# Optimization experiments

Hardware: AMD Instinct MI355X
Metric: run time of the kernel (lower is better)

## Reference

```python
import jax, jax.numpy as jnp
import numpy as np

MARGIN = 5.0
VAR_FLOOR = 1e-4
BIG = 1e6


def setup_inputs() -> dict:
    key = jax.random.key(0)
    ks = jax.random.split(key, 8)
    B, D, R = 512, 768, 128
    C_new, C_old = 10, 100
    return {
        "features": jax.random.normal(ks[0], (B, D), jnp.float32),
        "labels": jax.random.randint(ks[1], (B,), 0, C_new),
        "new_class_ids": jnp.arange(C_new),
        "cur_means": jax.random.normal(ks[2], (C_new, D), jnp.float32),
        "cur_bases": jax.random.normal(ks[3], (C_new, D, R), jnp.float32),
        "cur_variances": jax.random.uniform(ks[4], (C_new, R + 1), jnp.float32),
        "calibrated_old_means": jax.random.normal(ks[5], (C_old, D), jnp.float32),
        "calibrated_old_bases": jax.random.normal(ks[6], (C_old, D, R), jnp.float32),
        "calibrated_old_variances": jax.random.uniform(ks[7], (C_old, R + 1), jnp.float32),
    }


def _geometry_distance_matrix(z, means, bases, variances):
    # z: [B,D], means: [C,D], bases: [C,D,R], variances: [C,R+1] -> [B,C]
    diff = z[:, None, :] - means[None, :, :]                    # [B,C,D]
    coeff = jnp.einsum('bcd,cdr->bcr', diff, bases)             # [B,C,R]
    eig = jnp.maximum(variances[:, :-1], VAR_FLOOR)             # [C,R]
    res = jnp.maximum(variances[:, -1], VAR_FLOOR)              # [C]
    parallel = jnp.sum(coeff * coeff / eig[None, :, :], axis=-1)  # [B,C]
    recon = jnp.einsum('bcr,cdr->bcd', coeff, bases)            # [B,C,D]
    residual_term = jnp.sum((diff - recon) ** 2, axis=-1) / res[None, :]
    dist = (parallel + residual_term) / z.shape[1]              # normalize_by_dim
    return jnp.nan_to_num(dist, nan=BIG, posinf=BIG, neginf=BIG)


def reference(features, labels, new_class_ids, cur_means, cur_bases, cur_variances,
              calibrated_old_means, calibrated_old_bases, calibrated_old_variances):
    z = jnp.nan_to_num(features, nan=0.0, posinf=0.0, neginf=0.0)  # [B,D]
    labels = labels.reshape(-1)

    own_all = _geometry_distance_matrix(z, cur_means, cur_bases, cur_variances)  # [B,C_new_total]
    old_all = _geometry_distance_matrix(z, calibrated_old_means, calibrated_old_bases,
                                        calibrated_old_variances)               # [B,C_old]
    old_min = jnp.min(old_all, axis=1)                                           # [B]

    # Per-new-class masks; union of class masks reproduces new_mask implicitly.
    masks = (labels[None, :] == new_class_ids[:, None]).astype(z.dtype)          # [K,B]
    counts = masks.sum(axis=1)                                                   # [K]
    denom = jnp.maximum(counts, 1.0)

    own_k = own_all[:, new_class_ids].T                                          # [K,B]
    hinge = jax.nn.relu(MARGIN + own_k - old_min[None, :])                       # [K,B]

    total_k = (hinge * masks).sum(axis=1) / denom
    own_k_mean = (own_k * masks).sum(axis=1) / denom
    old_k_mean = (old_min[None, :] * masks).sum(axis=1) / denom

    valid = (counts > 0).astype(z.dtype)
    n_valid = jnp.maximum(valid.sum(), 1.0)
    total = (total_k * valid).sum() / n_valid
    own = (own_k_mean * valid).sum() / n_valid
    old = (old_k_mean * valid).sum() / n_valid
    return jnp.stack([total, own, old])  # [total, own, old]
```

## Files before the change

kernel.cpp:

```cpp
#include <hip/hip_runtime.h>
#include <hip/hip_bf16.h>
#include <math.h>
#include <stdint.h>

#define B_N   512
#define D_N   768
#define R_N   128
#define C_NEW 10
#define C_OLD 100
#define C_TOT 110
#define MARGIN_F    5.0f
#define VAR_FLOOR_F 1e-4f
#define BIG_F       1e6f

typedef __bf16 bf16;
typedef __bf16 bf16x4 __attribute__((ext_vector_type(4)));
typedef __bf16 bf16x8 __attribute__((ext_vector_type(8)));
typedef float  f32x4  __attribute__((ext_vector_type(4)));

__device__ __forceinline__ float cleanf(float v) { return isfinite(v) ? v : 0.0f; }

__device__ __forceinline__ void gld16(const bf16* g, bf16* l) {
    __builtin_amdgcn_global_load_lds(
        (const __attribute__((address_space(1))) unsigned int*)g,
        (__attribute__((address_space(3))) unsigned int*)l, 16, 0, 0);
}

__global__ __launch_bounds__(256)
void prep_z(const float* __restrict__ z, bf16* __restrict__ zbf, float* __restrict__ znorm)
{
    const int wave = threadIdx.x >> 6, lane = threadIdx.x & 63;
    const int b = blockIdx.x * 4 + wave;
    const float4* src = (const float4*)(z + (size_t)b * D_N);
    bf16x4* dst = (bf16x4*)(zbf + (size_t)b * D_N);
    float nrm = 0.f;
    #pragma unroll
    for (int i = 0; i < 3; ++i) {
        float4 v = src[lane + i * 64];
        v.x = cleanf(v.x); v.y = cleanf(v.y); v.z = cleanf(v.z); v.w = cleanf(v.w);
        nrm += v.x * v.x + v.y * v.y + v.z * v.z + v.w * v.w;
        bf16x4 w;
        w[0] = (bf16)v.x; w[1] = (bf16)v.y; w[2] = (bf16)v.z; w[3] = (bf16)v.w;
        dst[lane + i * 64] = w;
    }
    #pragma unroll
    for (int off = 32; off >= 1; off >>= 1) nrm += __shfl_xor(nrm, off, 64);
    if (lane == 0) znorm[b] = nrm;
}

__global__ __launch_bounds__(256)
void prep_bases(const float* __restrict__ cur_bases, const float* __restrict__ old_bases,
                const float* __restrict__ cur_means, const float* __restrict__ old_means,
                bf16* __restrict__ basesT, bf16* __restrict__ G,
                float* __restrict__ m_c, float* __restrict__ munorm)
{
    const int c = blockIdx.x;
    const float* Bc = (c < C_NEW) ? cur_bases + (size_t)c * D_N * R_N
                                  : old_bases + (size_t)(c - C_NEW) * D_N * R_N;
    const float* mu = (c < C_NEW) ? cur_means + (size_t)c * D_N
                                  : old_means + (size_t)(c - C_NEW) * D_N;

    __shared__ bf16 T[128][136];
    __shared__ float sMu[D_N];
    __shared__ float sRed[256];

    const int tid = threadIdx.x, wave = tid >> 6, lane = tid & 63;
    const int quad = lane >> 4, l15 = lane & 15;
    const int wr = (wave >> 1) * 64, wcn = (wave & 1) * 64;

    float mn = 0.f;
    for (int i = tid; i < D_N; i += 256) { float v = mu[i]; sMu[i] = v; mn += v * v; }
    #pragma unroll
    for (int off = 32; off >= 1; off >>= 1) mn += __shfl_xor(mn, off, 64);
    if (lane == 0) sRed[wave] = mn;
    __syncthreads();
    if (tid == 0) munorm[c] = sRed[0] + sRed[1] + sRed[2] + sRed[3];

    float mcAcc = 0.f;
    const int mr = tid & 127, mdh = tid >> 7;

    f32x4 acc[4][4];
    #pragma unroll
    for (int i = 0; i < 4; ++i)
        #pragma unroll
        for (int j = 0; j < 4; ++j) acc[i][j] = (f32x4)0.0f;

    for (int ch = 0; ch < 6; ++ch) {
        const int d0 = ch * 128;
        __syncthreads();
        #pragma unroll
        for (int m = 0; m < 2; ++m) {
            int u = m * 256 + tid;
            int r4 = (u & 31) * 4;
            int dg = u >> 5;
            float4 v[8];
            #pragma unroll
            for (int j = 0; j < 8; ++j)
                v[j] = *(const float4*)(Bc + (size_t)(d0 + dg * 8 + j) * R_N + r4);
            #pragma unroll
            for (int i = 0; i < 4; ++i) {
                bf16x8 w;
                #pragma unroll
                for (int j = 0; j < 8; ++j) {
                    float f = (i == 0) ? v[j].x : (i == 1) ? v[j].y : (i == 2) ? v[j].z : v[j].w;
                    w[j] = (bf16)f;
                }
                *(bf16x8*)&T[r4 + i][dg * 8] = w;
            }
        }
        __syncthreads();
        {
            int r = tid >> 1, hf = tid & 1;
            const uint4* srcp = (const uint4*)&T[r][hf * 64];
            uint4* dstp = (uint4*)(basesT + (size_t)c * R_N * D_N + (size_t)r * D_N + d0 + hf * 64);
            #pragma unroll
            for (int m2 = 0; m2 < 8; ++m2) dstp[m2] = srcp[m2];
        }
        #pragma unroll 8
        for (int k = 0; k < 64; ++k)
            mcAcc += sMu[d0 + mdh * 64 + k] * (float)T[mr][mdh * 64 + k];
        #pragma unroll
        for (int kk = 0; kk < 128; kk += 32) {
            bf16x8 af[4], bg[4];
            #pragma unroll
            for (int i = 0; i < 4; ++i) af[i] = *(const bf16x8*)&T[wr + 16 * i + l15][kk + quad * 8];
            #pragma unroll
            for (int j = 0; j < 4; ++j) bg[j] = *(const bf16x8*)&T[wcn + 16 * j + l15][kk + quad * 8];
            #pragma unroll
            for (int i = 0; i < 4; ++i)
                #pragma unroll
                for (int j = 0; j < 4; ++j)
                    acc[i][j] = __builtin_amdgcn_mfma_f32_16x16x32_bf16(af[i], bg[j], acc[i][j], 0, 0, 0);
        }
    }
    __syncthreads();
    sRed[tid] = mcAcc;
    __syncthreads();
    if (tid < 128) m_c[c * R_N + tid] = sRed[tid] + sRed[128 + tid];

    #pragma unroll
    for (int i = 0; i < 4; ++i)
        #pragma unroll
        for (int j = 0; j < 4; ++j)
            #pragma unroll
            for (int reg = 0; reg < 4; ++reg) {
                int r = wr + 16 * i + quad * 4 + reg;
                int s = wcn + 16 * j + l15;
                G[(size_t)c * 16384 + (size_t)r * 128 + s] = (bf16)acc[i][j][reg];
            }
}

#define PADC 136
#define SM_AB  0
#define SM_C   32768
#define SM_M   67584
#define SM_INV 68096
#define SM_PAR 68608
#define SM_CN  69120
#define SM_Q   69632
#define SM_T2  70144
#define SM_MU  73216
#define SM_SZ  74752

__global__ __launch_bounds__(256, 2)
void main_dist(const bf16* __restrict__ zbf, const bf16* __restrict__ basesT,
               const bf16* __restrict__ G, const float* __restrict__ m_c,
               const float* __restrict__ cur_vars, const float* __restrict__ old_vars,
               const float* __restrict__ cur_means, const float* __restrict__ old_means,
               const float* __restrict__ znorm, const float* __restrict__ munorm,
               float* __restrict__ gdist)
{
    const int mt = blockIdx.x, c = blockIdx.y;
    const int b0 = mt * 128;
    const float* vars = (c < C_NEW) ? cur_vars + (size_t)c * (R_N + 1)
                                    : old_vars + (size_t)(c - C_NEW) * (R_N + 1);
    const float* mu = (c < C_NEW) ? cur_means + (size_t)c * D_N
                                  : old_means + (size_t)(c - C_NEW) * D_N;
    __shared__ __align__(16) unsigned char smem[SM_SZ];
    bf16*  sA   = (bf16*)(smem + SM_AB);
    bf16*  sB   = (bf16*)(smem + SM_AB + 16384);
    bf16*  sG   = (bf16*)(smem + SM_AB);
    bf16*  sC   = (bf16*)(smem + SM_C);
    float* sM   = (float*)(smem + SM_M);
    float* sInv = (float*)(smem + SM_INV);
    float* sPar = (float*)(smem + SM_PAR);
    float* sCn  = (float*)(smem + SM_CN);
    float* sQ   = (float*)(smem + SM_Q);
    float* sT2  = (float*)(smem + SM_T2);
    bf16*  sMuB = (bf16*)(smem + SM_MU);

    const int tid = threadIdx.x, wave = tid >> 6, lane = tid & 63;
    const int quad = lane >> 4, l15 = lane & 15;
    const int wr = (wave >> 1) * 64, wc = (wave & 1) * 64;

    if (tid < 128) {
        sM[tid]   = m_c[c * R_N + tid];
        sInv[tid] = 1.0f / fmaxf(vars[tid], VAR_FLOOR_F);
        sQ[tid]   = 0.0f;
    }
    for (int i = tid; i < D_N; i += 256) sMuB[i] = (bf16)mu[i];

    f32x4 acc1[4][4];
    #pragma unroll
    for (int i = 0; i < 4; ++i)
        #pragma unroll
        for (int j = 0; j < 4; ++j) acc1[i][j] = (f32x4)0.0f;
    float zd = 0.f;
    const int zrow = tid >> 1, zhalf = tid & 1;

    const bf16* Az = zbf + (size_t)b0 * D_N;
    const bf16* Bb = basesT + (size_t)c * R_N * D_N;
    const int rl = lane >> 3;
    const int cl = lane & 7;

    for (int k0 = 0; k0 < D_N; k0 += 64) {
        __syncthreads();
        #pragma unroll
        for (int j = 0; j < 4; ++j) {
            int r0 = j * 32 + wave * 8;
            gld16(Az + (size_t)(r0 + rl) * D_N + k0 + cl * 8, sA + r0 * 64);
            gld16(Bb + (size_t)(r0 + rl) * D_N + k0 + cl * 8, sB + r0 * 64);
        }
        __syncthreads();
        #pragma unroll
        for (int kk = 0; kk < 64; kk += 32) {
            bf16x8 af[4], bg[4];
            #pragma unroll
            for (int i = 0; i < 4; ++i) af[i] = *(const bf16x8*)(sA + (wr + 16 * i + l15) * 64 + kk + quad * 8);
            #pragma unroll
            for (int j = 0; j < 4; ++j) bg[j] = *(const bf16x8*)(sB + (wc + 16 * j + l15) * 64 + kk + quad * 8);
            #pragma unroll
            for (int i = 0; i < 4; ++i)
                #pragma unroll
                for (int j = 0; j < 4; ++j)
                    acc1[i][j] = __builtin_amdgcn_mfma_f32_16x16x32_bf16(af[i], bg[j], acc1[i][j], 0, 0, 0);
        }
        {
            const bf16* zr = sA + zrow * 64 + zhalf * 32;
            const bf16* mr = sMuB + k0 + zhalf * 32;
            #pragma unroll
            for (int m = 0; m < 4; ++m) {
                bf16x8 a = *(const bf16x8*)(zr + m * 8);
                bf16x8 b = *(const bf16x8*)(mr + m * 8);
                #pragma unroll
                for (int e = 0; e < 8; ++e) zd += (float)a[e] * (float)b[e];
            }
        }
    }
    sT2[512 + tid] = zd;

    #pragma unroll
    for (int j = 0; j < 4; ++j) {
        float mcv = sM[wc + 16 * j + l15];
        #pragma unroll
        for (int i = 0; i < 4; ++i)
            #pragma unroll
            for (int reg = 0; reg < 4; ++reg) {
                float cv = acc1[i][j][reg] - mcv;
                acc1[i][j][reg] = cv;
                int row = wr + 16 * i + quad * 4 + reg;
                int col = wc + 16 * j + l15;
                sC[row * PADC + col] = (bf16)cv;
            }
    }
    __syncthreads();

    {
        int row = tid >> 1, half = tid & 1;
        float par = 0.f, cn = 0.f;
        #pragma unroll
        for (int m = 0; m < 8; ++m) {
            bf16x8 v = *(const bf16x8*)(sC + row * PADC + half * 64 + m * 8);
            #pragma unroll
            for (int e = 0; e < 8; ++e) {
                float f = (float)v[e];
                int col = half * 64 + m * 8 + e;
                cn  += f * f;
                par += f * f * sInv[col];
            }
        }
        sT2[tid] = par;
        sT2[256 + tid] = cn;
    }
    {
        const bf16* Gc = G + (size_t)c * 16384;
        #pragma unroll
        for (int j = 0; j < 8; ++j) {
            int off = (wave * 8 + j) * 512;
            gld16(Gc + off + lane * 8, sG + off);
        }
    }
    __syncthreads();
    if (tid < 128) {
        sPar[tid] = sT2[tid * 2] + sT2[tid * 2 + 1];
        sCn[tid]  = sT2[256 + tid * 2] + sT2[256 + tid * 2 + 1];
    }

    f32x4 acc2[4][4];
    #pragma unroll
    for (int i = 0; i < 4; ++i)
        #pragma unroll
        for (int j = 0; j < 4; ++j) acc2[i][j] = (f32x4)0.0f;
    #pragma unroll
    for (int kc = 0; kc < 128; kc += 32) {
        bf16x8 af[4], bg[4];
        #pragma unroll
        for (int i = 0; i < 4; ++i) af[i] = *(const bf16x8*)(sC + (wr + 16 * i + l15) * PADC + kc + quad * 8);
        #pragma unroll
        for (int j = 0; j < 4; ++j) bg[j] = *(const bf16x8*)(sG + (wc + 16 * j + l15) * 128 + kc + quad * 8);
        #pragma unroll
        for (int i = 0; i < 4; ++i)
            #pragma unroll
            for (int j = 0; j < 4; ++j)
                acc2[i][j] = __builtin_amdgcn_mfma_f32_16x16x32_bf16(af[i], bg[j], acc2[i][j], 0, 0, 0);
    }

    #pragma unroll
    for (int i = 0; i < 4; ++i)
        #pragma unroll
        for (int reg = 0; reg < 4; ++reg) {
            float qp = 0.f;
            #pragma unroll
            for (int j = 0; j < 4; ++j) qp += acc2[i][j][reg] * acc1[i][j][reg];
            qp += __shfl_xor(qp, 1, 64);
            qp += __shfl_xor(qp, 2, 64);
            qp += __shfl_xor(qp, 4, 64);
            qp += __shfl_xor(qp, 8, 64);
            if (l15 == 0) atomicAdd(&sQ[wr + 16 * i + quad * 4 + reg], qp);
        }
    __syncthreads();

    if (tid < 128) {
        int b = b0 + tid;
        float zdot = sT2[512 + tid * 2] + sT2[512 + tid * 2 + 1];
        float nd2 = znorm[b] - 2.0f * zdot + munorm[c];
        float res = fmaxf(vars[R_N], VAR_FLOOR_F);
        float dist = (sPar[tid] + (nd2 - 2.0f * sCn[tid] + sQ[tid]) / res) / (float)D_N;
        if (!isfinite(dist)) dist = BIG_F;
        gdist[(size_t)b * C_TOT + c] = dist;
    }
}

__global__ __launch_bounds__(64)
void finalize_stage1(const float* __restrict__ gdist,
                     const int* __restrict__ labels,
                     const int* __restrict__ ncid,
                     float* __restrict__ acc)
{
    const int b = blockIdx.x * 64 + threadIdx.x;
    const float* row = gdist + (size_t)b * C_TOT;
    float mn = 3.4e38f;
    #pragma unroll
    for (int cc = C_NEW; cc < C_TOT; ++cc) mn = fminf(mn, row[cc]);
    const int lab = labels[b];
    #pragma unroll
    for (int k = 0; k < C_NEW; ++k) {
        if (lab == ncid[k]) {
            int col = min(max(ncid[k], 0), C_TOT - 1);
            float ow = row[col];
            atomicAdd(&acc[k * 4 + 0], 1.0f);
            atomicAdd(&acc[k * 4 + 1], fmaxf(0.0f, MARGIN_F + ow - mn));
            atomicAdd(&acc[k * 4 + 2], ow);
            atomicAdd(&acc[k * 4 + 3], mn);
        }
    }
}

__global__ __launch_bounds__(64)
void finalize_stage2(const float* __restrict__ acc, float* __restrict__ out)
{
    if (threadIdx.x == 0) {
        float total = 0.f, own = 0.f, old = 0.f, nv = 0.f;
        #pragma unroll
        for (int k = 0; k < C_NEW; ++k) {
            float cnt = acc[k * 4 + 0];
            float den = fmaxf(cnt, 1.0f);
            if (cnt > 0.f) {
                nv += 1.f;
                total += acc[k * 4 + 1] / den;
                own   += acc[k * 4 + 2] / den;
                old   += acc[k * 4 + 3] / den;
            }
        }
        float nvd = fmaxf(nv, 1.0f);
        out[0] = total / nvd;
        out[1] = own / nvd;
        out[2] = old / nvd;
    }
}

extern "C" void kernel_launch(void* const* d_in, const int* in_sizes, int n_in,
                              void* d_out, int out_size, void* d_ws, size_t ws_size,
                              hipStream_t stream)
{
    const float* features  = (const float*)d_in[0];
    const int*   labels    = (const int*)d_in[1];
    const int*   ncid      = (const int*)d_in[2];
    const float* cur_means = (const float*)d_in[3];
    const float* cur_bases = (const float*)d_in[4];
    const float* cur_vars  = (const float*)d_in[5];
    const float* old_means = (const float*)d_in[6];
    const float* old_bases = (const float*)d_in[7];
    const float* old_vars  = (const float*)d_in[8];

    unsigned char* ws = (unsigned char*)d_ws;
    float* gdist  = (float*)(ws + 0);
    bf16*  zbf    = (bf16*) (ws + 225280);
    float* znorm  = (float*)(ws + 1011712);
    float* munorm = (float*)(ws + 1013760);
    float* m_c    = (float*)(ws + 1014272);
    float* acc    = (float*)(ws + 1070592);
    bf16*  basesT = (bf16*) (ws + 1070848);
    bf16*  G      = (bf16*) (ws + 22697728);

    hipMemsetAsync(acc, 0, 256, stream);

    prep_z<<<dim3(128), dim3(256), 0, stream>>>(features, zbf, znorm);
    prep_bases<<<dim3(C_TOT), dim3(256), 0, stream>>>(cur_bases, old_bases,
                                                      cur_means, old_means,
                                                      basesT, G, m_c, munorm);
    main_dist<<<dim3(4, C_TOT), dim3(256), 0, stream>>>(zbf, basesT, G, m_c,
                                                        cur_vars, old_vars,
                                                        cur_means, old_means,
                                                        znorm, munorm, gdist);
    finalize_stage1<<<dim3(8), dim3(64), 0, stream>>>(gdist, labels, ncid, acc);
    finalize_stage2<<<dim3(1), dim3(64), 0, stream>>>(acc, (float*)d_out);
}
```

Before: 170.1 us.

## Split per-class basis prep across three D-chunks and fuse prep and finalize kernels

Merges prep_z and prep_bases into one launch and splits each class's basis preprocessing into three blocks over D-chunks. Partial Gram matrices, m_c and munorm are combined with global float atomics into fp32 buffers that are zeroed by one memset. main_dist now reads the fp32 Gram and converts it to bf16 itself. The two finalize kernels become one single-block kernel that reduces with shared-memory atomics. The aim is more parallelism in the 110-block prep stage and fewer launches, at the cost of about 1.8M global atomics, a larger memset and nondeterministic summation order.

```diff
diff --git a/kernel.cpp b/kernel.cpp
--- a/kernel.cpp
+++ b/kernel.cpp
@@ -27,54 +27,60 @@
 }
 
 __global__ __launch_bounds__(256)
-void prep_z(const float* __restrict__ z, bf16* __restrict__ zbf, float* __restrict__ znorm)
-{
-    const int wave = threadIdx.x >> 6, lane = threadIdx.x & 63;
-    const int b = blockIdx.x * 4 + wave;
-    const float4* src = (const float4*)(z + (size_t)b * D_N);
-    bf16x4* dst = (bf16x4*)(zbf + (size_t)b * D_N);
-    float nrm = 0.f;
-    #pragma unroll
-    for (int i = 0; i < 3; ++i) {
-        float4 v = src[lane + i * 64];
-        v.x = cleanf(v.x); v.y = cleanf(v.y); v.z = cleanf(v.z); v.w = cleanf(v.w);
-        nrm += v.x * v.x + v.y * v.y + v.z * v.z + v.w * v.w;
-        bf16x4 w;
-        w[0] = (bf16)v.x; w[1] = (bf16)v.y; w[2] = (bf16)v.z; w[3] = (bf16)v.w;
-        dst[lane + i * 64] = w;
-    }
-    #pragma unroll
-    for (int off = 32; off >= 1; off >>= 1) nrm += __shfl_xor(nrm, off, 64);
-    if (lane == 0) znorm[b] = nrm;
-}
-
-__global__ __launch_bounds__(256)
-void prep_bases(const float* __restrict__ cur_bases, const float* __restrict__ old_bases,
+void prep_fused(const float* __restrict__ z,
+                const float* __restrict__ cur_bases, const float* __restrict__ old_bases,
                 const float* __restrict__ cur_means, const float* __restrict__ old_means,
-                bf16* __restrict__ basesT, bf16* __restrict__ G,
+                bf16* __restrict__ zbf, float* __restrict__ znorm,
+                bf16* __restrict__ basesT, float* __restrict__ Gacc,
                 float* __restrict__ m_c, float* __restrict__ munorm)
 {
-    const int c = blockIdx.x;
+    const int tid = threadIdx.x, wave = tid >> 6, lane = tid & 63;
+
+    if (blockIdx.x < 128) {
+        const int b = blockIdx.x * 4 + wave;
+        const float4* src = (const float4*)(z + (size_t)b * D_N);
+        bf16x4* dst = (bf16x4*)(zbf + (size_t)b * D_N);
+        float nrm = 0.f;
+        #pragma unroll
+        for (int i = 0; i < 3; ++i) {
+            float4 v = src[lane + i * 64];
+            v.x = cleanf(v.x); v.y = cleanf(v.y); v.z = cleanf(v.z); v.w = cleanf(v.w);
+            nrm += v.x * v.x + v.y * v.y + v.z * v.z + v.w * v.w;
+            bf16x4 w;
+            w[0] = (bf16)v.x; w[1] = (bf16)v.y; w[2] = (bf16)v.z; w[3] = (bf16)v.w;
+            dst[lane + i * 64] = w;
+        }
+        #pragma unroll
+        for (int off = 32; off >= 1; off >>= 1) nrm += __shfl_xor(nrm, off, 64);
+        if (lane == 0) znorm[b] = nrm;
+        return;
+    }
+
+    const int pb = blockIdx.x - 128;
+    const int c = pb / 3, part = pb % 3;
     const float* Bc = (c < C_NEW) ? cur_bases + (size_t)c * D_N * R_N
                                   : old_bases + (size_t)(c - C_NEW) * D_N * R_N;
     const float* mu = (c < C_NEW) ? cur_means + (size_t)c * D_N
                                   : old_means + (size_t)(c - C_NEW) * D_N;
 
     __shared__ bf16 T[128][136];
-    __shared__ float sMu[D_N];
+    __shared__ float sMu[256];
     __shared__ float sRed[256];
 
-    const int tid = threadIdx.x, wave = tid >> 6, lane = tid & 63;
     const int quad = lane >> 4, l15 = lane & 15;
     const int wr = (wave >> 1) * 64, wcn = (wave & 1) * 64;
-
-    float mn = 0.f;
-    for (int i = tid; i < D_N; i += 256) { float v = mu[i]; sMu[i] = v; mn += v * v; }
-    #pragma unroll
-    for (int off = 32; off >= 1; off >>= 1) mn += __shfl_xor(mn, off, 64);
-    if (lane == 0) sRed[wave] = mn;
-    __syncthreads();
-    if (tid == 0) munorm[c] = sRed[0] + sRed[1] + sRed[2] + sRed[3];
+    const int dbase = part * 256;
+
+    {
+        float v = mu[dbase + tid];
+        sMu[tid] = v;
+        float mn = v * v;
+        #pragma unroll
+        for (int off = 32; off >= 1; off >>= 1) mn += __shfl_xor(mn, off, 64);
+        if (lane == 0) sRed[wave] = mn;
+    }
+    __syncthreads();
+    if (tid == 0) atomicAdd(&munorm[c], sRed[0] + sRed[1] + sRed[2] + sRed[3]);
 
     float mcAcc = 0.f;
     const int mr = tid & 127, mdh = tid >> 7;
@@ -85,8 +91,8 @@
         #pragma unroll
         for (int j = 0; j < 4; ++j) acc[i][j] = (f32x4)0.0f;
 
-    for (int ch = 0; ch < 6; ++ch) {
-        const int d0 = ch * 128;
+    for (int ch = 0; ch < 2; ++ch) {
+        const int d0 = dbase + ch * 128;
         __syncthreads();
         #pragma unroll
         for (int m = 0; m < 2; ++m) {
@@ -118,7 +124,7 @@
         }
         #pragma unroll 8
         for (int k = 0; k < 64; ++k)
-            mcAcc += sMu[d0 + mdh * 64 + k] * (float)T[mr][mdh * 64 + k];
+            mcAcc += sMu[ch * 128 + mdh * 64 + k] * (float)T[mr][mdh * 64 + k];
         #pragma unroll
         for (int kk = 0; kk < 128; kk += 32) {
             bf16x8 af[4], bg[4];
@@ -136,7 +142,7 @@
     __syncthreads();
     sRed[tid] = mcAcc;
     __syncthreads();
-    if (tid < 128) m_c[c * R_N + tid] = sRed[tid] + sRed[128 + tid];
+    if (tid < 128) atomicAdd(&m_c[c * R_N + tid], sRed[tid] + sRed[128 + tid]);
 
     #pragma unroll
     for (int i = 0; i < 4; ++i)
@@ -146,7 +152,7 @@
             for (int reg = 0; reg < 4; ++reg) {
                 int r = wr + 16 * i + quad * 4 + reg;
                 int s = wcn + 16 * j + l15;
-                G[(size_t)c * 16384 + (size_t)r * 128 + s] = (bf16)acc[i][j][reg];
+                atomicAdd(&Gacc[(size_t)c * 16384 + (size_t)r * 128 + s], acc[i][j][reg]);
             }
 }
 
@@ -164,7 +170,7 @@
 
 __global__ __launch_bounds__(256, 2)
 void main_dist(const bf16* __restrict__ zbf, const bf16* __restrict__ basesT,
-               const bf16* __restrict__ G, const float* __restrict__ m_c,
+               const float* __restrict__ Gacc, const float* __restrict__ m_c,
                const float* __restrict__ cur_vars, const float* __restrict__ old_vars,
                const float* __restrict__ cur_means, const float* __restrict__ old_means,
                const float* __restrict__ znorm, const float* __restrict__ munorm,
@@ -283,11 +289,14 @@
         sT2[256 + tid] = cn;
     }
     {
-        const bf16* Gc = G + (size_t)c * 16384;
-        #pragma unroll
-        for (int j = 0; j < 8; ++j) {
-            int off = (wave * 8 + j) * 512;
-            gld16(Gc + off + lane * 8, sG + off);
+        const float* Gc = Gacc + (size_t)c * 16384;
+        #pragma unroll
+        for (int m = 0; m < 16; ++m) {
+            int idx = (m * 256 + tid) * 4;
+            float4 v = *(const float4*)(Gc + idx);
+            bf16x4 w;
+            w[0] = (bf16)v.x; w[1] = (bf16)v.y; w[2] = (bf16)v.z; w[3] = (bf16)v.w;
+            *(bf16x4*)(sG + idx) = w;
         }
     }
     __syncthreads();
@@ -341,45 +350,45 @@
     }
 }
 
-__global__ __launch_bounds__(64)
-void finalize_stage1(const float* __restrict__ gdist,
-                     const int* __restrict__ labels,
-                     const int* __restrict__ ncid,
-                     float* __restrict__ acc)
+__global__ __launch_bounds__(512)
+void finalize(const float* __restrict__ gdist,
+              const int* __restrict__ labels,
+              const int* __restrict__ ncid,
+              float* __restrict__ out)
 {
-    const int b = blockIdx.x * 64 + threadIdx.x;
-    const float* row = gdist + (size_t)b * C_TOT;
+    __shared__ float sAcc[C_NEW * 4];
+    const int tid = threadIdx.x;
+    if (tid < C_NEW * 4) sAcc[tid] = 0.f;
+    __syncthreads();
+
+    const float* row = gdist + (size_t)tid * C_TOT;
     float mn = 3.4e38f;
     #pragma unroll
     for (int cc = C_NEW; cc < C_TOT; ++cc) mn = fminf(mn, row[cc]);
-    const int lab = labels[b];
+    const int lab = labels[tid];
     #pragma unroll
     for (int k = 0; k < C_NEW; ++k) {
         if (lab == ncid[k]) {
             int col = min(max(ncid[k], 0), C_TOT - 1);
             float ow = row[col];
-            atomicAdd(&acc[k * 4 + 0], 1.0f);
-            atomicAdd(&acc[k * 4 + 1], fmaxf(0.0f, MARGIN_F + ow - mn));
-            atomicAdd(&acc[k * 4 + 2], ow);
-            atomicAdd(&acc[k * 4 + 3], mn);
-        }
-    }
-}
-
-__global__ __launch_bounds__(64)
-void finalize_stage2(const float* __restrict__ acc, float* __restrict__ out)
-{
-    if (threadIdx.x == 0) {
+            atomicAdd(&sAcc[k * 4 + 0], 1.0f);
+            atomicAdd(&sAcc[k * 4 + 1], fmaxf(0.0f, MARGIN_F + ow - mn));
+            atomicAdd(&sAcc[k * 4 + 2], ow);
+            atomicAdd(&sAcc[k * 4 + 3], mn);
+        }
+    }
+    __syncthreads();
+    if (tid == 0) {
         float total = 0.f, own = 0.f, old = 0.f, nv = 0.f;
         #pragma unroll
         for (int k = 0; k < C_NEW; ++k) {
-            float cnt = acc[k * 4 + 0];
+            float cnt = sAcc[k * 4 + 0];
             float den = fmaxf(cnt, 1.0f);
             if (cnt > 0.f) {
                 nv += 1.f;
-                total += acc[k * 4 + 1] / den;
-                own   += acc[k * 4 + 2] / den;
-                old   += acc[k * 4 + 3] / den;
+                total += sAcc[k * 4 + 1] / den;
+                own   += sAcc[k * 4 + 2] / den;
+                old   += sAcc[k * 4 + 3] / den;
             }
         }
         float nvd = fmaxf(nv, 1.0f);
@@ -409,20 +418,17 @@
     float* znorm  = (float*)(ws + 1011712);
     float* munorm = (float*)(ws + 1013760);
     float* m_c    = (float*)(ws + 1014272);
-    float* acc    = (float*)(ws + 1070592);
-    bf16*  basesT = (bf16*) (ws + 1070848);
-    bf16*  G      = (bf16*) (ws + 22697728);
-
-    hipMemsetAsync(acc, 0, 256, stream);
-
-    prep_z<<<dim3(128), dim3(256), 0, stream>>>(features, zbf, znorm);
-    prep_bases<<<dim3(C_TOT), dim3(256), 0, stream>>>(cur_bases, old_bases,
-                                                      cur_means, old_means,
-                                                      basesT, G, m_c, munorm);
-    main_dist<<<dim3(4, C_TOT), dim3(256), 0, stream>>>(zbf, basesT, G, m_c,
+    float* Gacc   = (float*)(ws + 1070592);
+    bf16*  basesT = (bf16*) (ws + 8279552);
+
+    hipMemsetAsync(munorm, 0, 512 + 56320 + 7208960, stream);
+
+    prep_fused<<<dim3(128 + 3 * C_TOT), dim3(256), 0, stream>>>(
+        features, cur_bases, old_bases, cur_means, old_means,
+        zbf, znorm, basesT, Gacc, m_c, munorm);
+    main_dist<<<dim3(4, C_TOT), dim3(256), 0, stream>>>(zbf, basesT, Gacc, m_c,
                                                         cur_vars, old_vars,
                                                         cur_means, old_means,
                                                         znorm, munorm, gdist);
-    finalize_stage1<<<dim3(8), dim3(64), 0, stream>>>(gdist, labels, ncid, acc);
-    finalize_stage2<<<dim3(1), dim3(64), 0, stream>>>(acc, (float*)d_out);
+    finalize<<<dim3(1), dim3(512), 0, stream>>>(gdist, labels, ncid, (float*)d_out);
 }
```

Result: no change. 172.5 us (+1.4%).
